# Performance work log

Measured on AMD Instinct MI355X. Metric: run time of the kernel, lower is better.

## Reference

```python
import jax, jax.numpy as jnp
import numpy as np

OBS_RADIUS = 1.0
N = 8192      # num_agents
IN_DIM = 4    # state dim: [x, y, vx, vy]
HID = 64


def setup_inputs() -> dict:
    key = jax.random.key(0)
    ks = jax.random.split(key, 6)
    states = jax.random.normal(ks[0], (N, IN_DIM), dtype=jnp.float32)
    W1 = jax.random.normal(ks[1], (IN_DIM, HID), dtype=jnp.float32) / np.sqrt(IN_DIM).astype(np.float32)
    b1 = jnp.zeros((HID,), jnp.float32)
    W2 = jax.random.normal(ks[2], (HID, HID), dtype=jnp.float32) / np.sqrt(HID).astype(np.float32)
    b2 = jnp.zeros((HID,), jnp.float32)
    cw = jax.random.normal(ks[3], (HID,), dtype=jnp.float32) / np.sqrt(HID).astype(np.float32)  # Conv1d(64,1,1) weight
    cb = jnp.zeros((1,), jnp.float32)
    return {"states": states, "W1": W1, "b1": b1, "W2": W2, "b2": b2, "cw": cw, "cb": cb}


def _build_norm_adj(states):
    # radius graph on first two coords (positions); no self edges in the edge list,
    # GCNConv then adds self-loops and does symmetric D^-1/2 (A+I) D^-1/2 normalization.
    pos = states[:, :2]
    d2 = jnp.sum((pos[:, None, :] - pos[None, :, :]) ** 2, axis=-1)  # [N, N]
    mask = d2 <= jnp.asarray(OBS_RADIUS ** 2, states.dtype)          # [N, N] bool (incl. diagonal)
    eye = jnp.eye(N, dtype=bool)
    A_hat = jnp.where(mask & ~eye, jnp.asarray(1.0, states.dtype), 0.0) + jnp.eye(N, dtype=states.dtype)
    dinv = jax.lax.rsqrt(jnp.sum(A_hat, axis=1))                     # deg >= 1 (self loop)
    A_norm = dinv[:, None] * A_hat * dinv[None, :]
    return A_norm, mask


def reference(states, W1, b1, W2, b2, cw, cb):
    A_norm, mask = _build_norm_adj(states)
    # GCNConv 1: aggregate(normalized adj) of X W, plus bias, ReLU
    h = jax.nn.relu(A_norm @ (states @ W1) + b1)   # [N, 64]
    # GCNConv 2
    h = jax.nn.relu(A_norm @ (h @ W2) + b2)        # [N, 64]
    # Conv1d(64 -> 1, kernel=1): pointwise linear over channels
    out = h @ cw[:, None] + cb                     # [N, 1]
    return out, mask
```

## Files before the change

kernel.cpp:

```cpp
#include <hip/hip_runtime.h>
#include <hip/hip_bf16.h>
#include <stdint.h>

#define NPTS 8192
#define KSPLIT 16

typedef float f32x4 __attribute__((ext_vector_type(4)));
typedef short s16x8 __attribute__((ext_vector_type(8)));

__device__ __forceinline__ unsigned short f2bf(float f) {
    unsigned int u = __builtin_bit_cast(unsigned int, f);
    u += 0x7FFFu + ((u >> 16) & 1u);
    return (unsigned short)(u >> 16);
}


__global__ __launch_bounds__(256) void k_mask(const float* __restrict__ states,
                                              const float* __restrict__ W1,
                                              float* __restrict__ mout,
                                              unsigned long long* __restrict__ maskb,
                                              float* __restrict__ dinv,
                                              uint4* __restrict__ y1) {
    __shared__ float xs[NPTS];
    __shared__ float ys[NPTS];
    __shared__ float dls[16];
    int tid = threadIdx.x;
    for (int r = tid; r < NPTS; r += 256) {
        float4 s = ((const float4*)states)[r];
        xs[r] = s.x; ys[r] = s.y;
    }
    __syncthreads();
    int wv = tid >> 6, L = tid & 63;
    int rowbase = blockIdx.x * 16 + wv * 4;
    float xi[4], yi[4];
    int deg[4] = {0, 0, 0, 0};
#pragma unroll
    for (int rr = 0; rr < 4; ++rr) { xi[rr] = xs[rowbase + rr]; yi[rr] = ys[rowbase + rr]; }
    for (int it = 0; it < 128; ++it) {
        int j = it * 64 + L;
        float xj = xs[j], yj = ys[j];
#pragma unroll
        for (int rr = 0; rr < 4; ++rr) {
            float dx = xi[rr] - xj;
            float dy = yi[rr] - yj;
            float d2 = __fadd_rn(__fmul_rn(dx, dx), __fmul_rn(dy, dy));
            bool pred = (d2 <= 1.0f);
            __builtin_nontemporal_store(pred ? 1.0f : 0.0f,
                                        &mout[(size_t)(rowbase + rr) * NPTS + j]);
            unsigned long long b = __ballot(pred);
            if (L == 0) maskb[(size_t)(rowbase + rr) * 128 + it] = b;
            deg[rr] += (int)__popcll(b);
        }
    }
    if (L == 0) {
#pragma unroll
        for (int rr = 0; rr < 4; ++rr) {
            float dv = rsqrtf((float)deg[rr]);
            dinv[rowbase + rr] = dv;
            dls[wv * 4 + rr] = dv;
        }
    }
    __syncthreads();
    if (tid < 128) {
        int ql = tid >> 6;
        int ct = (tid >> 4) & 3;
        int nn = tid & 15;
        int col = ct * 16 + nn;
        float w0 = W1[col], w1 = W1[64 + col], w2 = W1[128 + col], w3 = W1[192 + col];
        unsigned short frag[8];
#pragma unroll
        for (int t = 0; t < 8; ++t) {
            int rloc = ql * 8 + t;
            int k = blockIdx.x * 16 + rloc;
            float4 s = ((const float4*)states)[k];
            float acc = s.x * w0 + s.y * w1 + s.z * w2 + s.w * w3;
            frag[t] = f2bf(dls[rloc] * acc);
        }
        uint4 u;
        u.x = (unsigned)frag[0] | ((unsigned)frag[1] << 16);
        u.y = (unsigned)frag[2] | ((unsigned)frag[3] << 16);
        u.z = (unsigned)frag[4] | ((unsigned)frag[5] << 16);
        u.w = (unsigned)frag[6] | ((unsigned)frag[7] << 16);
        int kb = blockIdx.x >> 1;
        int quad = ql + 2 * (blockIdx.x & 1);
        y1[(kb * 4 + ct) * 64 + quad * 16 + nn] = u;
    }
}

__global__ __launch_bounds__(256) void k_agg(const uint4* __restrict__ y,
                                             const unsigned int* __restrict__ maskb,
                                             float* __restrict__ zp) {
    int tid = threadIdx.x;
    int wv = tid >> 6, L = tid & 63;
    int mt = blockIdx.x >> 4, ks = blockIdx.x & (KSPLIT - 1);
    int n = L & 15, quad = L >> 4;
    int i0 = mt * 256 + wv * 64 + n;
    const unsigned int* mrow0 = maskb + (size_t)i0 * 256 + ks * 16;
    const unsigned int* mrow1 = mrow0 + 16 * 256;
    const unsigned int* mrow2 = mrow0 + 32 * 256;
    const unsigned int* mrow3 = mrow0 + 48 * 256;
    const uint4* yb = y + (size_t)(ks * 16) * 256 + L;

    f32x4 acc[4][4] = {{{0,0,0,0},{0,0,0,0},{0,0,0,0},{0,0,0,0}},
                       {{0,0,0,0},{0,0,0,0},{0,0,0,0},{0,0,0,0}},
                       {{0,0,0,0},{0,0,0,0},{0,0,0,0},{0,0,0,0}},
                       {{0,0,0,0},{0,0,0,0},{0,0,0,0},{0,0,0,0}}};
    uint4 bcur[4];
    unsigned int mw0 = mrow0[0], mw1 = mrow1[0], mw2 = mrow2[0], mw3 = mrow3[0];
#pragma unroll
    for (int ct = 0; ct < 4; ++ct) bcur[ct] = yb[ct * 64];

    for (int kb = 0; kb < 16; ++kb) {
        uint4 bnext[4];
        unsigned int mwn0 = 0, mwn1 = 0, mwn2 = 0, mwn3 = 0;
        if (kb < 15) {
            const uint4* p = yb + (kb + 1) * 256;
#pragma unroll
            for (int ct = 0; ct < 4; ++ct) bnext[ct] = p[ct * 64];
            mwn0 = mrow0[kb + 1]; mwn1 = mrow1[kb + 1];
            mwn2 = mrow2[kb + 1]; mwn3 = mrow3[kb + 1];
        }
        unsigned int by0 = (mw0 >> (quad * 8)) & 0xFFu;
        unsigned int by1 = (mw1 >> (quad * 8)) & 0xFFu;
        unsigned int by2 = (mw2 >> (quad * 8)) & 0xFFu;
        unsigned int by3 = (mw3 >> (quad * 8)) & 0xFFu;
        s16x8 a0, a1, a2, a3;
#pragma unroll
        for (int t = 0; t < 8; ++t) {
            a0[t] = (short)(((by0 >> t) & 1u) ? 0x3F80 : 0);
            a1[t] = (short)(((by1 >> t) & 1u) ? 0x3F80 : 0);
            a2[t] = (short)(((by2 >> t) & 1u) ? 0x3F80 : 0);
            a3[t] = (short)(((by3 >> t) & 1u) ? 0x3F80 : 0);
        }
#pragma unroll
        for (int ct = 0; ct < 4; ++ct) {
            s16x8 b = __builtin_bit_cast(s16x8, bcur[ct]);
            acc[0][ct] = __builtin_amdgcn_mfma_f32_16x16x32_bf16(a0, b, acc[0][ct], 0, 0, 0);
            acc[1][ct] = __builtin_amdgcn_mfma_f32_16x16x32_bf16(a1, b, acc[1][ct], 0, 0, 0);
            acc[2][ct] = __builtin_amdgcn_mfma_f32_16x16x32_bf16(a2, b, acc[2][ct], 0, 0, 0);
            acc[3][ct] = __builtin_amdgcn_mfma_f32_16x16x32_bf16(a3, b, acc[3][ct], 0, 0, 0);
        }
#pragma unroll
        for (int ct = 0; ct < 4; ++ct) bcur[ct] = bnext[ct];
        mw0 = mwn0; mw1 = mwn1; mw2 = mwn2; mw3 = mwn3;
    }
    float* zb = zp + (size_t)ks * (NPTS * 64) + (size_t)(mt * 256 + wv * 64) * 64;
#pragma unroll
    for (int g = 0; g < 4; ++g)
#pragma unroll
        for (int ct = 0; ct < 4; ++ct)
#pragma unroll
            for (int r = 0; r < 4; ++r)
                zb[(g * 16 + quad * 4 + r) * 64 + ct * 16 + n] = acc[g][ct][r];
}

__global__ __launch_bounds__(256) void k_h1y2(const float* __restrict__ zp,
                                              const float* __restrict__ dinv,
                                              const float* __restrict__ b1,
                                              const float* __restrict__ W2,
                                              uint4* __restrict__ y2) {
    __shared__ float w2s[4096];
    __shared__ float hbuf[8 * 64];
    __shared__ unsigned short ybuf[8 * 64];
    int tid = threadIdx.x;
#pragma unroll
    for (int s = 0; s < 16; ++s) w2s[s * 256 + tid] = W2[s * 256 + tid];
    int j0 = blockIdx.x * 8;
#pragma unroll
    for (int e = tid; e < 512; e += 256) {
        int r = e >> 6, c = e & 63;
        int j = j0 + r;
        float z = 0.0f;
#pragma unroll
        for (int s = 0; s < KSPLIT; ++s) z += zp[(size_t)s * (NPTS * 64) + j * 64 + c];
        hbuf[r * 64 + c] = fmaxf(dinv[j] * z + b1[c], 0.0f);
    }
    __syncthreads();
#pragma unroll
    for (int e = tid; e < 512; e += 256) {
        int r = e >> 6, c = e & 63;
        const float* hr = hbuf + r * 64;
        float acc = 0.0f;
#pragma unroll
        for (int m = 0; m < 64; ++m) acc = fmaf(hr[m], w2s[m * 64 + c], acc);
        ybuf[r * 64 + c] = f2bf(dinv[j0 + r] * acc);
    }
    __syncthreads();
    if (tid < 64) {
        int c = tid;
        unsigned short v[8];
#pragma unroll
        for (int r = 0; r < 8; ++r) v[r] = ybuf[r * 64 + c];
        uint4 u;
        u.x = (unsigned)v[0] | ((unsigned)v[1] << 16);
        u.y = (unsigned)v[2] | ((unsigned)v[3] << 16);
        u.z = (unsigned)v[4] | ((unsigned)v[5] << 16);
        u.w = (unsigned)v[6] | ((unsigned)v[7] << 16);
        int kb = j0 >> 5, quad = (j0 >> 3) & 3, ct = c >> 4, nn = c & 15;
        y2[(kb * 4 + ct) * 64 + quad * 16 + nn] = u;
    }
}

__global__ __launch_bounds__(256) void k_out(const float* __restrict__ zp,
                                             const float* __restrict__ dinv,
                                             const float* __restrict__ b2,
                                             const float* __restrict__ cw,
                                             const float* __restrict__ cb,
                                             float* __restrict__ out) {
    int tid = threadIdx.x;
    int wv = tid >> 6, L = tid & 63;
    int i = blockIdx.x * 4 + wv;
    int idx = i * 64 + L;
    float z = 0.0f;
#pragma unroll
    for (int s = 0; s < KSPLIT; ++s) z += zp[(size_t)s * (NPTS * 64) + idx];
    float h = fmaxf(dinv[i] * z + b2[L], 0.0f);
    float v = h * cw[L];
#pragma unroll
    for (int off = 32; off > 0; off >>= 1) v += __shfl_down(v, off, 64);
    if (L == 0) out[i] = v + cb[0];
}

extern "C" void kernel_launch(void* const* d_in, const int* in_sizes, int n_in,
                              void* d_out, int out_size, void* d_ws, size_t ws_size,
                              hipStream_t stream) {
    const float* states = (const float*)d_in[0];
    const float* W1 = (const float*)d_in[1];
    const float* b1 = (const float*)d_in[2];
    const float* W2 = (const float*)d_in[3];
    const float* b2 = (const float*)d_in[4];
    const float* cw = (const float*)d_in[5];
    const float* cb = (const float*)d_in[6];
    float* out = (float*)d_out;
    float* mout = out + NPTS;

    char* ws = (char*)d_ws;
    float* dinv               = (float*)(ws);
    unsigned long long* maskb = (unsigned long long*)(ws + (1 << 16));
    uint4* y1                 = (uint4*)(ws + (1 << 16) + (8 << 20));
    uint4* y2                 = (uint4*)(ws + (1 << 16) + (9 << 20));
    float* zp                 = (float*)(ws + (1 << 16) + (10 << 20));

    hipLaunchKernelGGL(k_mask, dim3(512), dim3(256), 0, stream,
                       states, W1, mout, maskb, dinv, y1);
    hipLaunchKernelGGL(k_agg,  dim3(32 * KSPLIT), dim3(256), 0, stream,
                       y1, (const unsigned int*)maskb, zp);
    hipLaunchKernelGGL(k_h1y2, dim3(1024), dim3(256), 0, stream, zp, dinv, b1, W2, y2);
    hipLaunchKernelGGL(k_agg,  dim3(32 * KSPLIT), dim3(256), 0, stream,
                       y2, (const unsigned int*)maskb, zp);
    hipLaunchKernelGGL(k_out,  dim3(2048), dim3(256), 0, stream, zp, dinv, b2, cw, cb, out);
}
```

Baseline: 373.6 us.

## Fuse split-K aggregation with epilogues using in-block LDS reduction

Replaces the split-K aggregation kernel, which wrote 16 partial sums per row to global memory, with block-level kernels in which 8 waves each cover a K slice and reduce through shared memory. The layer-1 epilogue (bias, ReLU, W2 multiply, bf16 pack) and the layer-2 epilogue (bias, ReLU, final dot product) are fused into those kernels. This removes the large global partial-sum traffic and two kernel launches. In exchange there are only 256 blocks of 512 threads using about 75KB of LDS each, which limits occupancy, and each wave runs a longer serial K loop with fewer MFMA rows per mask load.

New measurement: 350.0 us. -6.3%, faster.

```diff
diff --git a/kernel.cpp b/kernel.cpp
--- a/kernel.cpp
+++ b/kernel.cpp
@@ -3,7 +3,6 @@
 #include <stdint.h>
 
 #define NPTS 8192
-#define KSPLIT 16
 
 typedef float f32x4 __attribute__((ext_vector_type(4)));
 typedef short s16x8 __attribute__((ext_vector_type(8)));
@@ -87,138 +86,134 @@
     }
 }
 
-__global__ __launch_bounds__(256) void k_agg(const uint4* __restrict__ y,
-                                             const unsigned int* __restrict__ maskb,
-                                             float* __restrict__ zp) {
-    int tid = threadIdx.x;
-    int wv = tid >> 6, L = tid & 63;
-    int mt = blockIdx.x >> 4, ks = blockIdx.x & (KSPLIT - 1);
+__device__ __forceinline__ void agg_core(const uint4* __restrict__ y,
+                                         const unsigned int* __restrict__ maskb,
+                                         const float* __restrict__ dinv,
+                                         const float* __restrict__ bias,
+                                         float* __restrict__ redbuf,
+                                         float* __restrict__ hbuf,
+                                         int R0) {
+    int tid = threadIdx.x;
+    int w = tid >> 6, L = tid & 63;
     int n = L & 15, quad = L >> 4;
-    int i0 = mt * 256 + wv * 64 + n;
-    const unsigned int* mrow0 = maskb + (size_t)i0 * 256 + ks * 16;
+    const unsigned int* mrow0 = maskb + (size_t)(R0 + n) * 256 + w * 32;
     const unsigned int* mrow1 = mrow0 + 16 * 256;
-    const unsigned int* mrow2 = mrow0 + 32 * 256;
-    const unsigned int* mrow3 = mrow0 + 48 * 256;
-    const uint4* yb = y + (size_t)(ks * 16) * 256 + L;
-
-    f32x4 acc[4][4] = {{{0,0,0,0},{0,0,0,0},{0,0,0,0},{0,0,0,0}},
-                       {{0,0,0,0},{0,0,0,0},{0,0,0,0},{0,0,0,0}},
-                       {{0,0,0,0},{0,0,0,0},{0,0,0,0},{0,0,0,0}},
+    const uint4* yb = y + (size_t)w * 8192 + L;
+
+    f32x4 acc[2][4] = {{{0,0,0,0},{0,0,0,0},{0,0,0,0},{0,0,0,0}},
                        {{0,0,0,0},{0,0,0,0},{0,0,0,0},{0,0,0,0}}};
     uint4 bcur[4];
-    unsigned int mw0 = mrow0[0], mw1 = mrow1[0], mw2 = mrow2[0], mw3 = mrow3[0];
+    unsigned int mw0 = mrow0[0], mw1 = mrow1[0];
 #pragma unroll
     for (int ct = 0; ct < 4; ++ct) bcur[ct] = yb[ct * 64];
 
-    for (int kb = 0; kb < 16; ++kb) {
+    for (int kk = 0; kk < 32; ++kk) {
         uint4 bnext[4];
-        unsigned int mwn0 = 0, mwn1 = 0, mwn2 = 0, mwn3 = 0;
-        if (kb < 15) {
-            const uint4* p = yb + (kb + 1) * 256;
+        unsigned int mwn0 = 0, mwn1 = 0;
+        if (kk < 31) {
+            const uint4* p = yb + (kk + 1) * 256;
 #pragma unroll
             for (int ct = 0; ct < 4; ++ct) bnext[ct] = p[ct * 64];
-            mwn0 = mrow0[kb + 1]; mwn1 = mrow1[kb + 1];
-            mwn2 = mrow2[kb + 1]; mwn3 = mrow3[kb + 1];
+            mwn0 = mrow0[kk + 1]; mwn1 = mrow1[kk + 1];
         }
         unsigned int by0 = (mw0 >> (quad * 8)) & 0xFFu;
         unsigned int by1 = (mw1 >> (quad * 8)) & 0xFFu;
-        unsigned int by2 = (mw2 >> (quad * 8)) & 0xFFu;
-        unsigned int by3 = (mw3 >> (quad * 8)) & 0xFFu;
-        s16x8 a0, a1, a2, a3;
+        s16x8 a0, a1;
 #pragma unroll
         for (int t = 0; t < 8; ++t) {
             a0[t] = (short)(((by0 >> t) & 1u) ? 0x3F80 : 0);
             a1[t] = (short)(((by1 >> t) & 1u) ? 0x3F80 : 0);
-            a2[t] = (short)(((by2 >> t) & 1u) ? 0x3F80 : 0);
-            a3[t] = (short)(((by3 >> t) & 1u) ? 0x3F80 : 0);
         }
 #pragma unroll
         for (int ct = 0; ct < 4; ++ct) {
             s16x8 b = __builtin_bit_cast(s16x8, bcur[ct]);
             acc[0][ct] = __builtin_amdgcn_mfma_f32_16x16x32_bf16(a0, b, acc[0][ct], 0, 0, 0);
             acc[1][ct] = __builtin_amdgcn_mfma_f32_16x16x32_bf16(a1, b, acc[1][ct], 0, 0, 0);
-            acc[2][ct] = __builtin_amdgcn_mfma_f32_16x16x32_bf16(a2, b, acc[2][ct], 0, 0, 0);
-            acc[3][ct] = __builtin_amdgcn_mfma_f32_16x16x32_bf16(a3, b, acc[3][ct], 0, 0, 0);
         }
 #pragma unroll
         for (int ct = 0; ct < 4; ++ct) bcur[ct] = bnext[ct];
-        mw0 = mwn0; mw1 = mwn1; mw2 = mwn2; mw3 = mwn3;
-    }
-    float* zb = zp + (size_t)ks * (NPTS * 64) + (size_t)(mt * 256 + wv * 64) * 64;
-#pragma unroll
-    for (int g = 0; g < 4; ++g)
+        mw0 = mwn0; mw1 = mwn1;
+    }
+    float* rb = redbuf + w * 2048;
+#pragma unroll
+    for (int g = 0; g < 2; ++g)
 #pragma unroll
         for (int ct = 0; ct < 4; ++ct)
 #pragma unroll
             for (int r = 0; r < 4; ++r)
-                zb[(g * 16 + quad * 4 + r) * 64 + ct * 16 + n] = acc[g][ct][r];
-}
-
-__global__ __launch_bounds__(256) void k_h1y2(const float* __restrict__ zp,
-                                              const float* __restrict__ dinv,
-                                              const float* __restrict__ b1,
-                                              const float* __restrict__ W2,
-                                              uint4* __restrict__ y2) {
+                rb[(g * 16 + quad * 4 + r) * 64 + ct * 16 + n] = acc[g][ct][r];
+    __syncthreads();
+    for (int e = tid; e < 2048; e += 512) {
+        float z = 0.0f;
+#pragma unroll
+        for (int ww = 0; ww < 8; ++ww) z += redbuf[ww * 2048 + e];
+        int row = e >> 6, col = e & 63;
+        hbuf[row * 66 + col] = fmaxf(dinv[R0 + row] * z + bias[col], 0.0f);
+    }
+    __syncthreads();
+}
+
+__global__ __launch_bounds__(512) void k_layer1(const uint4* __restrict__ y1,
+                                                const unsigned int* __restrict__ maskb,
+                                                const float* __restrict__ dinv,
+                                                const float* __restrict__ b1,
+                                                const float* __restrict__ W2,
+                                                uint4* __restrict__ y2) {
+    __shared__ float redbuf[8 * 2048];
+    __shared__ float hbuf[32 * 66];
     __shared__ float w2s[4096];
-    __shared__ float hbuf[8 * 64];
-    __shared__ unsigned short ybuf[8 * 64];
-    int tid = threadIdx.x;
-#pragma unroll
-    for (int s = 0; s < 16; ++s) w2s[s * 256 + tid] = W2[s * 256 + tid];
-    int j0 = blockIdx.x * 8;
-#pragma unroll
-    for (int e = tid; e < 512; e += 256) {
-        int r = e >> 6, c = e & 63;
-        int j = j0 + r;
-        float z = 0.0f;
-#pragma unroll
-        for (int s = 0; s < KSPLIT; ++s) z += zp[(size_t)s * (NPTS * 64) + j * 64 + c];
-        hbuf[r * 64 + c] = fmaxf(dinv[j] * z + b1[c], 0.0f);
-    }
-    __syncthreads();
-#pragma unroll
-    for (int e = tid; e < 512; e += 256) {
-        int r = e >> 6, c = e & 63;
-        const float* hr = hbuf + r * 64;
-        float acc = 0.0f;
-#pragma unroll
-        for (int m = 0; m < 64; ++m) acc = fmaf(hr[m], w2s[m * 64 + c], acc);
-        ybuf[r * 64 + c] = f2bf(dinv[j0 + r] * acc);
-    }
-    __syncthreads();
-    if (tid < 64) {
-        int c = tid;
+    int tid = threadIdx.x;
+    for (int s = tid; s < 4096; s += 512) w2s[s] = W2[s];
+    int R0 = blockIdx.x * 32;
+    agg_core(y1, maskb, dinv, b1, redbuf, hbuf, R0);
+    if (tid < 256) {
+        int nn = tid & 15, q = (tid >> 4) & 3, ct = tid >> 6;
+        int col = ct * 16 + nn;
+        float dot[8] = {0, 0, 0, 0, 0, 0, 0, 0};
+        for (int m = 0; m < 64; ++m) {
+            float wv = w2s[m * 64 + col];
+#pragma unroll
+            for (int t = 0; t < 8; ++t)
+                dot[t] = fmaf(hbuf[(q * 8 + t) * 66 + m], wv, dot[t]);
+        }
         unsigned short v[8];
 #pragma unroll
-        for (int r = 0; r < 8; ++r) v[r] = ybuf[r * 64 + c];
+        for (int t = 0; t < 8; ++t) v[t] = f2bf(dinv[R0 + q * 8 + t] * dot[t]);
         uint4 u;
         u.x = (unsigned)v[0] | ((unsigned)v[1] << 16);
         u.y = (unsigned)v[2] | ((unsigned)v[3] << 16);
         u.z = (unsigned)v[4] | ((unsigned)v[5] << 16);
         u.w = (unsigned)v[6] | ((unsigned)v[7] << 16);
-        int kb = j0 >> 5, quad = (j0 >> 3) & 3, ct = c >> 4, nn = c & 15;
-        y2[(kb * 4 + ct) * 64 + quad * 16 + nn] = u;
-    }
-}
-
-__global__ __launch_bounds__(256) void k_out(const float* __restrict__ zp,
-                                             const float* __restrict__ dinv,
-                                             const float* __restrict__ b2,
-                                             const float* __restrict__ cw,
-                                             const float* __restrict__ cb,
-                                             float* __restrict__ out) {
-    int tid = threadIdx.x;
-    int wv = tid >> 6, L = tid & 63;
-    int i = blockIdx.x * 4 + wv;
-    int idx = i * 64 + L;
-    float z = 0.0f;
-#pragma unroll
-    for (int s = 0; s < KSPLIT; ++s) z += zp[(size_t)s * (NPTS * 64) + idx];
-    float h = fmaxf(dinv[i] * z + b2[L], 0.0f);
-    float v = h * cw[L];
-#pragma unroll
-    for (int off = 32; off > 0; off >>= 1) v += __shfl_down(v, off, 64);
-    if (L == 0) out[i] = v + cb[0];
+        y2[(blockIdx.x * 4 + ct) * 64 + q * 16 + nn] = u;
+    }
+}
+
+__global__ __launch_bounds__(512) void k_layer2(const uint4* __restrict__ y2,
+                                                const unsigned int* __restrict__ maskb,
+                                                const float* __restrict__ dinv,
+                                                const float* __restrict__ b2,
+                                                const float* __restrict__ cw,
+                                                const float* __restrict__ cb,
+                                                float* __restrict__ out) {
+    __shared__ float redbuf[8 * 2048];
+    __shared__ float hbuf[32 * 66];
+    __shared__ float cws[64];
+    int tid = threadIdx.x;
+    if (tid < 64) cws[tid] = cw[tid];
+    int R0 = blockIdx.x * 32;
+    agg_core(y2, maskb, dinv, b2, redbuf, hbuf, R0);
+    int row = tid >> 4, cg = tid & 15;
+    float v = 0.0f;
+#pragma unroll
+    for (int e = 0; e < 4; ++e) {
+        int c = cg * 4 + e;
+        v = fmaf(hbuf[row * 66 + c], cws[c], v);
+    }
+    v += __shfl_down(v, 8);
+    v += __shfl_down(v, 4);
+    v += __shfl_down(v, 2);
+    v += __shfl_down(v, 1);
+    if (cg == 0) out[R0 + row] = v + cb[0];
 }
 
 extern "C" void kernel_launch(void* const* d_in, const int* in_sizes, int n_in,
@@ -239,14 +234,11 @@
     unsigned long long* maskb = (unsigned long long*)(ws + (1 << 16));
     uint4* y1                 = (uint4*)(ws + (1 << 16) + (8 << 20));
     uint4* y2                 = (uint4*)(ws + (1 << 16) + (9 << 20));
-    float* zp                 = (float*)(ws + (1 << 16) + (10 << 20));
-
-    hipLaunchKernelGGL(k_mask, dim3(512), dim3(256), 0, stream,
+
+    hipLaunchKernelGGL(k_mask,   dim3(512), dim3(256), 0, stream,
                        states, W1, mout, maskb, dinv, y1);
-    hipLaunchKernelGGL(k_agg,  dim3(32 * KSPLIT), dim3(256), 0, stream,
-                       y1, (const unsigned int*)maskb, zp);
-    hipLaunchKernelGGL(k_h1y2, dim3(1024), dim3(256), 0, stream, zp, dinv, b1, W2, y2);
-    hipLaunchKernelGGL(k_agg,  dim3(32 * KSPLIT), dim3(256), 0, stream,
-                       y2, (const unsigned int*)maskb, zp);
-    hipLaunchKernelGGL(k_out,  dim3(2048), dim3(256), 0, stream, zp, dinv, b2, cw, cb, out);
-}
+    hipLaunchKernelGGL(k_layer1, dim3(256), dim3(512), 0, stream,
+                       y1, (const unsigned int*)maskb, dinv, b1, W2, y2);
+    hipLaunchKernelGGL(k_layer2, dim3(256), dim3(512), 0, stream,
+                       y2, (const unsigned int*)maskb, dinv, b2, cw, cb, out);
+}
```
